# Optimization experiments

Hardware: AMD Instinct MI355X
Metric: run time of the kernel (lower is better)

The kernel has to match this reference:

```python
import jax, jax.numpy as jnp
import numpy as np

QMIN, QMAX = 0, 255        # 8-bit asymmetric activation quant bounds
GROUP_SIZE = 128

def setup_inputs() -> dict:
    key = jax.random.key(0)
    k1, k2, k3, k4, k5 = jax.random.split(key, 5)
    x = jax.random.normal(k1, (1, 2048, 4096), dtype=jnp.float32)
    qweight = jax.random.randint(k2, (4096, 32, 128), 0, 16, dtype=jnp.int32)  # uint4 codes
    w_scales = jax.random.uniform(k3, (4096, 32), dtype=jnp.float32, minval=0.001, maxval=0.02)
    w_zero_points = jax.random.randint(k4, (4096, 32), 0, 16, dtype=jnp.int32)
    bias = jax.random.normal(k5, (4096,), dtype=jnp.float32)
    return {"x": x, "qweight": qweight, "w_scales": w_scales,
            "w_zero_points": w_zero_points, "bias": bias}

def reference(x, qweight, w_scales, w_zero_points, bias):
    xf = x.astype(jnp.float32)
    # per-token (last-dim) asymmetric dynamic activation quantization
    xmin = jnp.min(xf, axis=-1, keepdims=True)
    xmax = jnp.max(xf, axis=-1, keepdims=True)
    x_scale = jnp.clip((xmax - xmin) / (QMAX - QMIN), 1e-5, None)
    x_zp = jnp.clip(jnp.round(-xmin / x_scale), QMIN, QMAX)
    q = jnp.clip(jnp.round(xf / x_scale) + x_zp, QMIN, QMAX)
    centered_x = (q - x_zp).reshape(*x.shape[:-1], -1, GROUP_SIZE)  # [B,S,G,C]
    # grouped weight dequant (zero-point centered)
    centered_w = qweight.astype(jnp.float32) - w_zero_points.astype(jnp.float32)[..., None]  # [O,G,C]
    acc = jnp.einsum('bsgc,ogc->bsog', centered_x, centered_w)  # [B,S,O,G]
    out = (acc * w_scales[None, None]).sum(axis=-1)  # apply per-group weight scales
    out = out * x_scale  # per-token activation scale
    out = out + bias
    return out
```

## Files before the change

### kernel.cpp

```cpp
#include <hip/hip_runtime.h>
#include <stdint.h>

#define M_DIM 2048
#define N_DIM 4096
#define K_DIM 4096
#define NGROUP 32
#define GSIZE 128

#define RQ_UP   (127.0f / 15.0f)
#define RQ_DOWN (15.0f / 127.0f)

#define BM 128
#define BN 256
#define NSLICE (K_DIM / 64)

typedef __attribute__((ext_vector_type(4))) int int32x4_t;

#define QUANT_BLOCKS M_DIM
#define DEQ_BLOCKS ((N_DIM * K_DIM) / 8 / 256)

__global__ __launch_bounds__(256) void prep_kernel(
        const float* __restrict__ x,
        const int* __restrict__ qw,
        const float* __restrict__ wsc,
        const int* __restrict__ wzp,
        char* __restrict__ A8,
        char* __restrict__ Bt8,
        float* __restrict__ xscale,
        float* __restrict__ xzpc,
        int* __restrict__ Sw)
{
    const int t = threadIdx.x;
    if (blockIdx.x < QUANT_BLOCKS) {
        const int s = blockIdx.x;
        const float* xrow = x + (size_t)s * K_DIM;

        float xv[16];
        float vmin = 1e38f, vmax = -1e38f;
#pragma unroll
        for (int p = 0; p < 4; ++p) {
            float4 v = *((const float4*)(xrow + p * 1024) + t);
            xv[p*4+0] = v.x; xv[p*4+1] = v.y; xv[p*4+2] = v.z; xv[p*4+3] = v.w;
            vmin = fminf(vmin, fminf(fminf(v.x, v.y), fminf(v.z, v.w)));
            vmax = fmaxf(vmax, fmaxf(fmaxf(v.x, v.y), fmaxf(v.z, v.w)));
        }
#pragma unroll
        for (int off = 32; off > 0; off >>= 1) {
            vmin = fminf(vmin, __shfl_xor(vmin, off));
            vmax = fmaxf(vmax, __shfl_xor(vmax, off));
        }
        __shared__ float smin[4], smax[4];
        const int wave = t >> 6;
        if ((t & 63) == 0) { smin[wave] = vmin; smax[wave] = vmax; }
        __syncthreads();
        vmin = fminf(fminf(smin[0], smin[1]), fminf(smin[2], smin[3]));
        vmax = fmaxf(fmaxf(smax[0], smax[1]), fmaxf(smax[2], smax[3]));

        float sc = (vmax - vmin) / 255.0f;
        sc = fmaxf(sc, 1e-5f);
        float zp = rintf(-vmin / sc);
        zp = fminf(fmaxf(zp, 0.0f), 255.0f);
        const float inv_sc = 1.0f / sc;

        const int r   = s & 127;
        const int mt  = s >> 7;
        const int swr = (r >> 1) & 3;
#pragma unroll
        for (int p = 0; p < 4; ++p) {
            int b[4];
#pragma unroll
            for (int e = 0; e < 4; ++e) {
                float q = fminf(fmaxf(rintf(xv[p*4+e] * inv_sc) + zp, 0.0f), 255.0f);
                b[e] = (int)q - 128;
            }
            unsigned pack = (b[0] & 0xff) | ((b[1] & 0xff) << 8) |
                            ((b[2] & 0xff) << 16) | ((b[3] & 0xff) << 24);
            const int kt   = p * 16 + (t >> 4);
            const int slot = ((t >> 2) & 3) ^ swr;
            *(unsigned*)(A8 + (((size_t)(mt * 64 + kt)) << 13)
                            + r * 64 + slot * 16 + (t & 3) * 4) = pack;
        }
        if (t == 0) { xscale[s] = sc; xzpc[s] = 128.0f - zp; }
    } else {
        const size_t base = ((size_t)(blockIdx.x - QUANT_BLOCKS) * 256 + t) * 8;
        const int n = (int)(base >> 12);
        const int g = (int)((base >> 7) & 31);
        const int zp = wzp[n * NGROUP + g];

        const int cl = t & 15;
        float2 wp = *(const float2*)(wsc + (size_t)n * NGROUP + cl * 2);
        float smx = fmaxf(wp.x, wp.y);
#pragma unroll
        for (int off = 1; off < 16; off <<= 1)
            smx = fmaxf(smx, __shfl_xor(smx, off));
        const float factor = wsc[n * NGROUP + g] * (RQ_UP / smx);

        int4 c0 = *(const int4*)(qw + base);
        int4 c1 = *(const int4*)(qw + base + 4);
        int w[8];
        w[0] = (int)rintf((float)(c0.x - zp) * factor);
        w[1] = (int)rintf((float)(c0.y - zp) * factor);
        w[2] = (int)rintf((float)(c0.z - zp) * factor);
        w[3] = (int)rintf((float)(c0.w - zp) * factor);
        w[4] = (int)rintf((float)(c1.x - zp) * factor);
        w[5] = (int)rintf((float)(c1.y - zp) * factor);
        w[6] = (int)rintf((float)(c1.z - zp) * factor);
        w[7] = (int)rintf((float)(c1.w - zp) * factor);
        uint2 pk;
        pk.x = (w[0] & 0xff) | ((w[1] & 0xff) << 8) | ((w[2] & 0xff) << 16) | ((w[3] & 0xff) << 24);
        pk.y = (w[4] & 0xff) | ((w[5] & 0xff) << 8) | ((w[6] & 0xff) << 16) | ((w[7] & 0xff) << 24);

        const int r  = n & 127;
        const int nt = n >> 7;
        const int kt = (int)((base >> 6) & 63);
        const int slot = (int)(((base >> 4) & 3)) ^ ((r >> 1) & 3);
        *(uint2*)(Bt8 + (((size_t)(nt * 64 + kt)) << 13)
                      + r * 64 + slot * 16 + (int)(base & 15)) = pk;

        int s8 = w[0] + w[1] + w[2] + w[3] + w[4] + w[5] + w[6] + w[7];
#pragma unroll
        for (int off = 1; off < 16; off <<= 1) s8 += __shfl_xor(s8, off);
        if ((t & 15) == 0)
            Sw[n * NGROUP + g] = s8;
    }
}

__global__ __launch_bounds__(256, 1) void gemm_kernel(
        const char* __restrict__ A8,
        const char* __restrict__ Bt8,
        const float* __restrict__ xscale,
        const float* __restrict__ xzpc,
        const float* __restrict__ wsc,
        const int* __restrict__ Sw,
        const float* __restrict__ bias,
        float* __restrict__ out)
{
    __shared__ float fws_s[BN], wsf_s[BN];

    const int tid  = threadIdx.x;
    const int bn   = blockIdx.x;
    const int bm   = blockIdx.y;
    const int wave = tid >> 6;
    const int lane = tid & 63;
    const int wr   = wave >> 1;
    const int wcl  = wave & 1;
    const int lrow  = lane & 15;
    const int lquad = lane >> 4;

    {
        const int n = bn * BN + tid;
        const int4* s4 = (const int4*)(Sw + (size_t)n * NGROUP);
        int acc = 0;
#pragma unroll
        for (int p = 0; p < 8; ++p) { int4 v = s4[p]; acc += v.x + v.y + v.z + v.w; }
        const float4* w4 = (const float4*)(wsc + (size_t)n * NGROUP);
        float s = 0.f;
#pragma unroll
        for (int p = 0; p < 8; ++p) {
            float4 w = w4[p];
            s = fmaxf(s, fmaxf(fmaxf(w.x, w.y), fmaxf(w.z, w.w)));
        }
        const float fw = s * RQ_DOWN;
        fws_s[tid] = fw;
        wsf_s[tid] = fw * (float)acc;
    }

    const int xq = (lquad ^ ((lrow >> 1) & 3)) * 16;
    const char* pA = A8 + ((size_t)bm << 19)
                        + (size_t)(wr * 64 + lrow) * 64 + xq;
    const char* pB = Bt8 + ((size_t)(bn * 2 + wcl) << 19)
                        + (size_t)lrow * 64 + xq;

    int32x4_t iacc[4][8];
    const int32x4_t zi = {0, 0, 0, 0};
#pragma unroll
    for (int i = 0; i < 4; ++i)
#pragma unroll
        for (int j = 0; j < 8; ++j) iacc[i][j] = zi;

#define LOADF(s, aF, bF) {                                            \
        const char* a_ = pA + ((size_t)(s) << 13);                    \
        const char* b_ = pB + ((size_t)(s) << 13);                    \
        _Pragma("unroll")                                             \
        for (int i_ = 0; i_ < 4; ++i_)                                \
            aF[i_] = *(const int32x4_t*)(a_ + i_ * 1024);             \
        _Pragma("unroll")                                             \
        for (int j_ = 0; j_ < 8; ++j_)                                \
            bF[j_] = *(const int32x4_t*)(b_ + j_ * 1024);             \
    }

#define MFMAS(aF, bF) {                                               \
        _Pragma("unroll")                                             \
        for (int i_ = 0; i_ < 4; ++i_)                                \
            _Pragma("unroll")                                         \
            for (int j_ = 0; j_ < 8; ++j_)                            \
                iacc[i_][j_] = __builtin_amdgcn_mfma_i32_16x16x64_i8( \
                    aF[i_], bF[j_], iacc[i_][j_], 0, 0, 0);           \
    }

    int32x4_t aX[4], bX[8], aY[4], bY[8];

    LOADF(0, aX, bX);
    LOADF(1, aY, bY);
#pragma unroll 1
    for (int s = 0; s < NSLICE - 2; s += 2) {
        MFMAS(aX, bX);
        LOADF(s + 2, aX, bX);
        MFMAS(aY, bY);
        LOADF(s + 3, aY, bY);
    }
    MFMAS(aX, bX);
    MFMAS(aY, bY);

    __syncthreads();

    float fn[8], wf[8], bb[8];
    int ncol[8];
#pragma unroll
    for (int j = 0; j < 8; ++j) {
        const int ncl = wcl * 128 + j * 16 + lrow;
        ncol[j] = bn * BN + ncl;
        fn[j] = fws_s[ncl];
        wf[j] = wsf_s[ncl];
        bb[j] = bias[ncol[j]];
    }
    const int m0 = bm * BM + wr * 64;
#pragma unroll
    for (int i = 0; i < 4; ++i) {
#pragma unroll
        for (int r = 0; r < 4; ++r) {
            const int m = m0 + i * 16 + lquad * 4 + r;
            const float xs  = xscale[m];
            const float czp = xzpc[m];
            float* orow = out + (size_t)m * N_DIM;
#pragma unroll
            for (int j = 0; j < 8; ++j)
                orow[ncol[j]] = xs * (fn[j] * (float)iacc[i][j][r] + czp * wf[j]) + bb[j];
        }
    }
#undef MFMAS
#undef LOADF
}

extern "C" void kernel_launch(void* const* d_in, const int* in_sizes, int n_in,
                              void* d_out, int out_size, void* d_ws, size_t ws_size,
                              hipStream_t stream) {
    const float* x     = (const float*)d_in[0];
    const int*   qw    = (const int*)d_in[1];
    const float* wsc   = (const float*)d_in[2];
    const int*   wzp   = (const int*)d_in[3];
    const float* bias  = (const float*)d_in[4];
    float* out = (float*)d_out;

    char* A8  = (char*)d_ws;
    char* Bt8 = A8 + (size_t)M_DIM * K_DIM;
    float* xscale = (float*)(Bt8 + (size_t)N_DIM * K_DIM);
    float* xzpc   = xscale + M_DIM;
    int*   Sw     = (int*)(xzpc + M_DIM);

    prep_kernel<<<QUANT_BLOCKS + DEQ_BLOCKS, 256, 0, stream>>>(
        x, qw, wsc, wzp, A8, Bt8, xscale, xzpc, Sw);

    dim3 grid(N_DIM / BN, M_DIM / BM);
    gemm_kernel<<<grid, 256, 0, stream>>>(
        A8, Bt8, xscale, xzpc, wsc, Sw, bias, out);
}
```

Measured before the change: 173.0 us.

## Triple-buffer GEMM register prefetch with inline-asm loads and explicit vmcnt waits

```diff
diff --git a/kernel.cpp b/kernel.cpp
--- a/kernel.cpp
+++ b/kernel.cpp
@@ -15,6 +15,14 @@
 #define NSLICE (K_DIM / 64)
 
 typedef __attribute__((ext_vector_type(4))) int int32x4_t;
+
+#define WAITVM_(N) asm volatile("s_waitcnt vmcnt(" #N ")")
+#define WAITVM(N)                                   \
+    do {                                            \
+        __builtin_amdgcn_sched_barrier(0);          \
+        WAITVM_(N);                                 \
+        __builtin_amdgcn_sched_barrier(0);          \
+    } while (0)
 
 #define QUANT_BLOCKS M_DIM
 #define DEQ_BLOCKS ((N_DIM * K_DIM) / 8 / 256)
@@ -164,6 +172,9 @@
         fws_s[tid] = fw;
         wsf_s[tid] = fw * (float)acc;
     }
+    __builtin_amdgcn_sched_barrier(0);
+    asm volatile("s_waitcnt vmcnt(0) lgkmcnt(0)");
+    __builtin_amdgcn_sched_barrier(0);
 
     const int xq = (lquad ^ ((lrow >> 1) & 3)) * 16;
     const char* pA = A8 + ((size_t)bm << 19)
@@ -179,14 +190,26 @@
         for (int j = 0; j < 8; ++j) iacc[i][j] = zi;
 
 #define LOADF(s, aF, bF) {                                            \
-        const char* a_ = pA + ((size_t)(s) << 13);                    \
-        const char* b_ = pB + ((size_t)(s) << 13);                    \
-        _Pragma("unroll")                                             \
-        for (int i_ = 0; i_ < 4; ++i_)                                \
-            aF[i_] = *(const int32x4_t*)(a_ + i_ * 1024);             \
-        _Pragma("unroll")                                             \
-        for (int j_ = 0; j_ < 8; ++j_)                                \
-            bF[j_] = *(const int32x4_t*)(b_ + j_ * 1024);             \
+        const char* a_  = pA + ((size_t)(s) << 13);                   \
+        const char* b0_ = pB + ((size_t)(s) << 13);                   \
+        const char* b1_ = b0_ + 4096;                                 \
+        asm volatile(                                                 \
+            "global_load_dwordx4 %0, %12, off\n\t"                    \
+            "global_load_dwordx4 %1, %12, off offset:1024\n\t"        \
+            "global_load_dwordx4 %2, %12, off offset:2048\n\t"        \
+            "global_load_dwordx4 %3, %12, off offset:3072\n\t"        \
+            "global_load_dwordx4 %4, %13, off\n\t"                    \
+            "global_load_dwordx4 %5, %13, off offset:1024\n\t"        \
+            "global_load_dwordx4 %6, %13, off offset:2048\n\t"        \
+            "global_load_dwordx4 %7, %13, off offset:3072\n\t"        \
+            "global_load_dwordx4 %8, %14, off\n\t"                    \
+            "global_load_dwordx4 %9, %14, off offset:1024\n\t"        \
+            "global_load_dwordx4 %10, %14, off offset:2048\n\t"       \
+            "global_load_dwordx4 %11, %14, off offset:3072"           \
+            : "=&v"(aF[0]), "=&v"(aF[1]), "=&v"(aF[2]), "=&v"(aF[3]), \
+              "=&v"(bF[0]), "=&v"(bF[1]), "=&v"(bF[2]), "=&v"(bF[3]), \
+              "=&v"(bF[4]), "=&v"(bF[5]), "=&v"(bF[6]), "=&v"(bF[7])  \
+            : "v"(a_), "v"(b0_), "v"(b1_));                           \
     }
 
 #define MFMAS(aF, bF) {                                               \
@@ -198,19 +221,21 @@
                     aF[i_], bF[j_], iacc[i_][j_], 0, 0, 0);           \
     }
 
-    int32x4_t aX[4], bX[8], aY[4], bY[8];
+    int32x4_t aX[4], bX[8], aY[4], bY[8], aZ[4], bZ[8];
 
     LOADF(0, aX, bX);
     LOADF(1, aY, bY);
+    LOADF(2, aZ, bZ);
 #pragma unroll 1
-    for (int s = 0; s < NSLICE - 2; s += 2) {
-        MFMAS(aX, bX);
-        LOADF(s + 2, aX, bX);
-        MFMAS(aY, bY);
-        LOADF(s + 3, aY, bY);
-    }
-    MFMAS(aX, bX);
-    MFMAS(aY, bY);
+    for (int s = 0; s < NSLICE - 4; s += 3) {
+        WAITVM(24); MFMAS(aX, bX); LOADF(s + 3, aX, bX);
+        WAITVM(24); MFMAS(aY, bY); LOADF(s + 4, aY, bY);
+        WAITVM(24); MFMAS(aZ, bZ); LOADF(s + 5, aZ, bZ);
+    }
+    WAITVM(24); MFMAS(aX, bX); LOADF(63, aX, bX);
+    WAITVM(24); MFMAS(aY, bY);
+    WAITVM(12); MFMAS(aZ, bZ);
+    WAITVM(0);  MFMAS(aX, bX);
 
     __syncthreads();
 
```

Measured after the change: 166.7 us. 3.6% less time.
